# Kernel optimization log

Hardware: AMD Instinct MI355X
Metric: run time of the kernel (lower is better)

## Reference

```python
import jax, jax.numpy as jnp
import numpy as np

HEAD_NUM = 16

def setup_inputs() -> dict:
    key = jax.random.key(0)
    k1, k2 = jax.random.split(key)
    bs, seq, d = 2, 2048, 1024
    embeddings = jax.random.normal(k1, (bs, seq, d), dtype=jnp.float32)
    W = jax.random.normal(k2, (d, 3 * d), dtype=jnp.float32) * (1.0 / np.sqrt(d))
    b = jnp.zeros((3 * d,), dtype=jnp.float32)
    return {"embeddings": embeddings, "W": W, "b": b}

def reference(embeddings, W, b):
    bs, seq, d = embeddings.shape
    h = HEAD_NUM
    qkv = embeddings @ W + b                      # [b, s, 3d]
    q, k, v = jnp.split(qkv, 3, axis=-1)          # each [b, s, d]
    hd = d // h
    # Faithful to source: reshape to (bs, seq, head_dim, heads) then permute
    def split_heads(x, head_dim):
        return x.reshape(bs, seq, head_dim, h).transpose(0, 3, 1, 2)  # [b, h, s, hd]
    mq = split_heads(q, hd)
    mk = split_heads(k, hd)
    mv = split_heads(v, hd)
    scale = jnp.sqrt(jnp.asarray(hd, dtype=mq.dtype))
    scores = jnp.einsum('bhqd,bhkd->bhqk', mq, mk) / scale  # [b, h, s, s]
    attn = jax.nn.softmax(scores, axis=-1)
    out = jnp.einsum('bhqk,bhkv->bhqv', attn, mv)            # [b, h, s, hd]
    return out.transpose(0, 2, 1, 3).reshape(bs, seq, -1)    # [b, s, d]
```

## Files before the change

kernel.cpp:

```cpp
#include <hip/hip_runtime.h>
#include <stdint.h>

typedef unsigned short u16;
typedef unsigned int u32;
typedef float f32x4 __attribute__((ext_vector_type(4)));
typedef __bf16 bf16x8 __attribute__((ext_vector_type(8)));

#define BS 2
#define SEQ 2048
#define DIM 1024
#define NW3 3072
#define NH 16
#define HD 64

#define MFMA_BF16(a, b, c) __builtin_amdgcn_mfma_f32_16x16x32_bf16((a), (b), (c), 0, 0, 0)

#define GLL16(g, l)                                                                \
  __builtin_amdgcn_global_load_lds(                                                \
      (__attribute__((address_space(1))) void*)(void*)(uintptr_t)(g),              \
      (__attribute__((address_space(3))) void*)(l), 16, 0, 0)

__device__ __forceinline__ float fexp2(float x) {
#if defined(__has_builtin)
#if __has_builtin(__builtin_amdgcn_exp2f)
  return __builtin_amdgcn_exp2f(x);
#else
  return exp2f(x);
#endif
#else
  return exp2f(x);
#endif
}

__device__ __forceinline__ u16 f2bf(float x) {
  __bf16 h = (__bf16)x;
  return __builtin_bit_cast(u16, h);
}

__global__ __launch_bounds__(256) void conv_a_kernel(const float* __restrict__ A,
                                                     u16* __restrict__ O) {
  int i = (blockIdx.x * 256 + threadIdx.x) * 4;
  float4 v = *(const float4*)(A + i);
  union { u16 u[4]; ushort4 v4; } p;
  p.u[0] = f2bf(v.x); p.u[1] = f2bf(v.y); p.u[2] = f2bf(v.z); p.u[3] = f2bf(v.w);
  *(ushort4*)(O + i) = p.v4;
}

__global__ __launch_bounds__(256) void conv_wt_kernel(const float* __restrict__ W,
                                                      u16* __restrict__ Wt) {
  int id = blockIdx.x * 256 + threadIdx.x;
  int kc = id / NW3;
  int n = id - kc * NW3;
  union { u16 u[8]; uint4 v; } p;
#pragma unroll
  for (int i = 0; i < 8; ++i) p.u[i] = f2bf(W[(kc * 8 + i) * NW3 + n]);
  int h = n & 15, hd = (n & 1023) >> 4;
  int np = (n & ~1023) + h * 64 + hd;
  *(uint4*)(Wt + np * DIM + kc * 8) = p.v;
}

__global__ __launch_bounds__(256) void gemm_qkv_kernel(
    const u16* __restrict__ Ab, const u16* __restrict__ Bt, const float* __restrict__ bias,
    u16* __restrict__ Q, u16* __restrict__ K, u16* __restrict__ Vt) {
  __shared__ __align__(16) u16 Al[128 * 64];
  __shared__ __align__(16) u16 Bl[128 * 64];
  const int t = threadIdx.x;
  const int lane = t & 63, wave = t >> 6;
  const int c = lane & 15, quad = lane >> 4;
  const int tm = blockIdx.x / 24, tn = blockIdx.x - tm * 24;
  const int wm = (wave >> 1) * 64, wn = (wave & 1) * 64;

  const char* Abase = (const char*)(Ab + (size_t)tm * 128 * DIM);
  const char* Bbase = (const char*)(Bt + (size_t)tn * 128 * DIM);

  f32x4 z = {0.f, 0.f, 0.f, 0.f};
  f32x4 acc[4][4];
#pragma unroll
  for (int i = 0; i < 4; ++i)
#pragma unroll
    for (int j = 0; j < 4; ++j) acc[i][j] = z;

  for (int kt = 0; kt < 16; ++kt) {
    __syncthreads();
    const int koff = kt * 128;
#pragma unroll
    for (int r = 0; r < 4; ++r) {
      int l = r * 256 + t;
      int row = l >> 3, pos = l & 7;
      int kc = pos ^ (row & 7);
      GLL16(Abase + row * 2048 + koff + kc * 16, (char*)Al + l * 16);
      GLL16(Bbase + row * 2048 + koff + kc * 16, (char*)Bl + l * 16);
    }
    __syncthreads();
#pragma unroll
    for (int ks = 0; ks < 2; ++ks) {
      bf16x8 af[4], bfr[4];
#pragma unroll
      for (int mt = 0; mt < 4; ++mt) {
        int row = wm + mt * 16 + c;
        int kc = (ks * 4 + quad) ^ (row & 7);
        af[mt] = *(const bf16x8*)((const char*)Al + row * 128 + kc * 16);
      }
#pragma unroll
      for (int nt = 0; nt < 4; ++nt) {
        int row = wn + nt * 16 + c;
        int kc = (ks * 4 + quad) ^ (row & 7);
        bfr[nt] = *(const bf16x8*)((const char*)Bl + row * 128 + kc * 16);
      }
#pragma unroll
      for (int mt = 0; mt < 4; ++mt)
#pragma unroll
        for (int nt = 0; nt < 4; ++nt)
          acc[mt][nt] = MFMA_BF16(af[mt], bfr[nt], acc[mt][nt]);
    }
  }

#pragma unroll
  for (int nt = 0; nt < 4; ++nt) {
    int np = tn * 128 + wn + nt * 16 + c;
    int which = np >> 10;
    int rem = np & 1023;
    int h = rem >> 6, hd = rem & 63;
    float bv = bias[(np & ~1023) + hd * 16 + h];
#pragma unroll
    for (int mt = 0; mt < 4; ++mt) {
      int mbase = tm * 128 + wm + mt * 16 + quad * 4;
      int bI = mbase >> 11;
      int s0 = mbase & 2047;
      if (which == 2) {
        union { u16 u[4]; uint2 v; } p;
#pragma unroll
        for (int r = 0; r < 4; ++r) p.u[r] = f2bf(acc[mt][nt][r] + bv);
        *(uint2*)(Vt + ((size_t)(bI * NH + h) * HD + hd) * SEQ + s0) = p.v;
      } else {
        u16* dst = (which == 0) ? Q : K;
#pragma unroll
        for (int r = 0; r < 4; ++r)
          dst[((size_t)(bI * NH + h) * SEQ + (s0 + r)) * HD + hd] = f2bf(acc[mt][nt][r] + bv);
      }
    }
  }
}

#define CSC 0.18033688011112042f

#define STAGE_KV(KDST, VDST, KTILE)                                            \
  {                                                                            \
    const char* Ktb = Kb + (size_t)(KTILE) * 8192;        \
    const char* Vtb = Vb + (size_t)(KTILE) * 128;         \
    _Pragma("unroll") for (int r = 0; r < 2; ++r) {                            \
      int l = r * 256 + t;                                                     \
      int row = l >> 3, pos = l & 7;                                           \
      int kc = pos ^ (row & 7);                                                \
      GLL16(Ktb + row * 128 + kc * 16, (char*)(KDST) + l * 16);                \
      GLL16(Vtb + row * 4096 + kc * 16, (char*)(VDST) + l * 16);               \
    }                                                                          \
  }

#define COMPUTE_TILE(KT, VT)                                                   \
  {                                                                            \
    f32x4 sT[4];                                                               \
    _Pragma("unroll") for (int mt = 0; mt < 4; ++mt) {                         \
      sT[mt] = z;                                                              \
      _Pragma("unroll") for (int ks = 0; ks < 2; ++ks) {                       \
        int row = mt * 16 + c;                                                 \
        int kc = (ks * 4 + quad) ^ (row & 7);                                  \
        bf16x8 kf = *(const bf16x8*)((const char*)(KT) + row * 128 + kc * 16); \
        sT[mt] = MFMA_BF16(kf, qf[ks], sT[mt]);                                \
      }                                                                        \
    }                                                                          \
    u32 pk[4][2];                                                              \
    _Pragma("unroll") for (int mt = 0; mt < 4; ++mt) {                         \
      float p0 = fexp2(sT[mt][0] * CSC);                                       \
      float p1 = fexp2(sT[mt][1] * CSC);                                       \
      float p2 = fexp2(sT[mt][2] * CSC);                                       \
      float p3 = fexp2(sT[mt][3] * CSC);                                       \
      sm0 += p0; sm1 += p1; sm2 += p2; sm3 += p3;                              \
      pk[mt][0] = (u32)f2bf(p0) | ((u32)f2bf(p1) << 16);                       \
      pk[mt][1] = (u32)f2bf(p2) | ((u32)f2bf(p3) << 16);                       \
    }                                                                          \
    _Pragma("unroll") for (int ks = 0; ks < 2; ++ks) {                         \
      u32 a0 = __shfl(pk[2 * ks][0], sl0), a1 = __shfl(pk[2 * ks][1], sl0);    \
      u32 a2 = __shfl(pk[2 * ks][0], sl1), a3 = __shfl(pk[2 * ks][1], sl1);    \
      u32 b0 = __shfl(pk[2 * ks + 1][0], sl0);                                 \
      u32 b1 = __shfl(pk[2 * ks + 1][1], sl0);                                 \
      u32 b2 = __shfl(pk[2 * ks + 1][0], sl1);                                 \
      u32 b3 = __shfl(pk[2 * ks + 1][1], sl1);                                 \
      uint4 wv;                                                                \
      wv.x = hi ? b0 : a0; wv.y = hi ? b1 : a1;                                \
      wv.z = hi ? b2 : a2; wv.w = hi ? b3 : a3;                                \
      bf16x8 pf = __builtin_bit_cast(bf16x8, wv);                              \
      _Pragma("unroll") for (int mt = 0; mt < 4; ++mt) {                       \
        int row = mt * 16 + c;                                                 \
        int kc = (ks * 4 + quad) ^ (row & 7);                                  \
        bf16x8 vf = *(const bf16x8*)((const char*)(VT) + row * 128 + kc * 16); \
        accO[mt] = MFMA_BF16(vf, pf, accO[mt]);                                \
      }                                                                        \
    }                                                                          \
  }

__global__ __launch_bounds__(256, 4) void attn_kernel(
    const u16* __restrict__ Q, const u16* __restrict__ K,
    const u16* __restrict__ Vt, float* __restrict__ Out) {
  __shared__ __align__(16) u16 Ka[64 * 64];
  __shared__ __align__(16) u16 Kb2[64 * 64];
  __shared__ __align__(16) u16 Va[64 * 64];
  __shared__ __align__(16) u16 Vb2[64 * 64];
  const int t = threadIdx.x;
  const int lane = t & 63, wave = t >> 6;
  const int c = lane & 15, quad = lane >> 4;
  const int qt = blockIdx.x & 31, bh = blockIdx.x >> 5;
  const int h = bh & 15, b = bh >> 4;

  const u16* Qb = Q + ((size_t)bh * SEQ + qt * 64) * HD;
  const char* Kb = (const char*)(K + (size_t)bh * SEQ * HD);
  const char* Vb = (const char*)(Vt + (size_t)bh * HD * SEQ);

#pragma unroll
  for (int r = 0; r < 2; ++r) {
    int l = r * 256 + t;
    int row = l >> 3, pos = l & 7;
    int kc = pos ^ (row & 7);
    GLL16((const char*)Qb + row * 128 + kc * 16, (char*)Ka + l * 16);
  }
  __syncthreads();
  bf16x8 qf[2];
#pragma unroll
  for (int ks = 0; ks < 2; ++ks) {
    int row = wave * 16 + c;
    int kc = (ks * 4 + quad) ^ (row & 7);
    qf[ks] = *(const bf16x8*)((const char*)Ka + row * 128 + kc * 16);
  }
  __syncthreads();

  float sm0 = 0.f, sm1 = 0.f, sm2 = 0.f, sm3 = 0.f;
  f32x4 z = {0.f, 0.f, 0.f, 0.f};
  f32x4 accO[4];
#pragma unroll
  for (int i = 0; i < 4; ++i) accO[i] = z;

  const int sl0 = c + 16 * ((quad & 1) * 2);
  const int sl1 = sl0 + 16;
  const bool hi = quad >= 2;

  STAGE_KV(Ka, Va, 0);
  __syncthreads();

  for (int kt = 0; kt < 32; kt += 2) {
    STAGE_KV(Kb2, Vb2, kt + 1);
    COMPUTE_TILE(Ka, Va);
    __syncthreads();
    if (kt + 2 < 32) STAGE_KV(Ka, Va, kt + 2);
    COMPUTE_TILE(Kb2, Vb2);
    __syncthreads();
  }

  float l = (sm0 + sm1) + (sm2 + sm3);
  l += __shfl_xor(l, 16);
  l += __shfl_xor(l, 32);
  float inv = 1.f / l;
  int s = qt * 64 + wave * 16 + c;
#pragma unroll
  for (int mt = 0; mt < 4; ++mt) {
    float4 o;
    o.x = accO[mt][0] * inv;
    o.y = accO[mt][1] * inv;
    o.z = accO[mt][2] * inv;
    o.w = accO[mt][3] * inv;
    size_t off = ((size_t)(b * SEQ + s)) * DIM + h * HD + mt * 16 + quad * 4;
    *(float4*)(Out + off) = o;
  }
}

extern "C" void kernel_launch(void* const* d_in, const int* in_sizes, int n_in,
                              void* d_out, int out_size, void* d_ws, size_t ws_size,
                              hipStream_t stream) {
  (void)in_sizes; (void)n_in; (void)out_size; (void)ws_size;
  const float* emb = (const float*)d_in[0];
  const float* W = (const float*)d_in[1];
  const float* bias = (const float*)d_in[2];
  float* out = (float*)d_out;
  char* ws = (char*)d_ws;
  u16* Ab = (u16*)ws;
  u16* Wt = (u16*)(ws + 8388608);
  u16* Qd = (u16*)(ws + 14680064);
  u16* Kd = (u16*)(ws + 23068672);
  u16* Vd = (u16*)(ws + 31457280);

  conv_a_kernel<<<4096, 256, 0, stream>>>(emb, Ab);
  conv_wt_kernel<<<1536, 256, 0, stream>>>(W, Wt);
  gemm_qkv_kernel<<<768, 256, 0, stream>>>(Ab, Wt, bias, Qd, Kd, Vd);
  attn_kernel<<<1024, 256, 0, stream>>>(Qd, Kd, Vd, out);
}
```

Before: 189.7 us.

## Double-buffer QKV GEMM tiles, fuse conversion kernels, fold softmax scale into Q

The QKV GEMM now uses two LDS buffers with a K-tile of 32 and issues the load of the next tile before computing the current one. This is meant to overlap global-to-LDS traffic with MFMA work, and it halves the per-stage tile size. The two fp32-to-bf16 conversion kernels are merged into a single launch to save one launch. The softmax scale is applied to Q in the GEMM epilogue, which removes a multiply per score in the attention inner loop but rounds the scaled Q to bf16.

```diff
diff --git a/kernel.cpp b/kernel.cpp
--- a/kernel.cpp
+++ b/kernel.cpp
@@ -37,33 +37,68 @@
   return __builtin_bit_cast(u16, h);
 }
 
-__global__ __launch_bounds__(256) void conv_a_kernel(const float* __restrict__ A,
-                                                     u16* __restrict__ O) {
-  int i = (blockIdx.x * 256 + threadIdx.x) * 4;
-  float4 v = *(const float4*)(A + i);
-  union { u16 u[4]; ushort4 v4; } p;
-  p.u[0] = f2bf(v.x); p.u[1] = f2bf(v.y); p.u[2] = f2bf(v.z); p.u[3] = f2bf(v.w);
-  *(ushort4*)(O + i) = p.v4;
-}
-
-__global__ __launch_bounds__(256) void conv_wt_kernel(const float* __restrict__ W,
-                                                      u16* __restrict__ Wt) {
-  int id = blockIdx.x * 256 + threadIdx.x;
-  int kc = id / NW3;
-  int n = id - kc * NW3;
-  union { u16 u[8]; uint4 v; } p;
-#pragma unroll
-  for (int i = 0; i < 8; ++i) p.u[i] = f2bf(W[(kc * 8 + i) * NW3 + n]);
-  int h = n & 15, hd = (n & 1023) >> 4;
-  int np = (n & ~1023) + h * 64 + hd;
-  *(uint4*)(Wt + np * DIM + kc * 8) = p.v;
-}
+#define CSC 0.18033688011112042f
+
+__global__ __launch_bounds__(256) void conv_kernel(const float* __restrict__ A,
+                                                   u16* __restrict__ O,
+                                                   const float* __restrict__ W,
+                                                   u16* __restrict__ Wt) {
+  if (blockIdx.x < 4096) {
+    int i = (blockIdx.x * 256 + threadIdx.x) * 4;
+    float4 v = *(const float4*)(A + i);
+    union { u16 u[4]; ushort4 v4; } p;
+    p.u[0] = f2bf(v.x); p.u[1] = f2bf(v.y); p.u[2] = f2bf(v.z); p.u[3] = f2bf(v.w);
+    *(ushort4*)(O + i) = p.v4;
+  } else {
+    int id = (blockIdx.x - 4096) * 256 + threadIdx.x;
+    int kc = id / NW3;
+    int n = id - kc * NW3;
+    union { u16 u[8]; uint4 v; } p;
+#pragma unroll
+    for (int i = 0; i < 8; ++i) p.u[i] = f2bf(W[(kc * 8 + i) * NW3 + n]);
+    int h = n & 15, hd = (n & 1023) >> 4;
+    int np = (n & ~1023) + h * 64 + hd;
+    *(uint4*)(Wt + np * DIM + kc * 8) = p.v;
+  }
+}
+
+#define GSTAGE(ADST, BDST, KT)                                                 \
+  {                                                                            \
+    const int koff = (KT) * 64;                                \
+    _Pragma("unroll") for (int r = 0; r < 2; ++r) {                            \
+      int l = r * 256 + t;                            \
+      int row = l >> 2, pos = l & 3;                                           \
+      int kc = pos ^ (row & 3);                                                \
+      GLL16(Abase + row * 2048 + koff + kc * 16, (char*)(ADST) + l * 16);      \
+      GLL16(Bbase + row * 2048 + koff + kc * 16, (char*)(BDST) + l * 16);      \
+    }                                                                          \
+  }
+
+#define GCOMPUTE(AT, BT)                                                       \
+  {                                                                            \
+    bf16x8 af[4], bfr[4];                                                      \
+    _Pragma("unroll") for (int mt = 0; mt < 4; ++mt) {                         \
+      int row = wm + mt * 16 + c;                                              \
+      int kc = quad ^ (row & 3);                                               \
+      af[mt] = *(const bf16x8*)((const char*)(AT) + row * 64 + kc * 16);       \
+    }                                                                          \
+    _Pragma("unroll") for (int nt = 0; nt < 4; ++nt) {                         \
+      int row = wn + nt * 16 + c;                                              \
+      int kc = quad ^ (row & 3);                                               \
+      bfr[nt] = *(const bf16x8*)((const char*)(BT) + row * 64 + kc * 16);      \
+    }                                                                          \
+    _Pragma("unroll") for (int mt = 0; mt < 4; ++mt)                           \
+      _Pragma("unroll") for (int nt = 0; nt < 4; ++nt)                         \
+        acc[mt][nt] = MFMA_BF16(af[mt], bfr[nt], acc[mt][nt]);                 \
+  }
 
 __global__ __launch_bounds__(256) void gemm_qkv_kernel(
     const u16* __restrict__ Ab, const u16* __restrict__ Bt, const float* __restrict__ bias,
     u16* __restrict__ Q, u16* __restrict__ K, u16* __restrict__ Vt) {
-  __shared__ __align__(16) u16 Al[128 * 64];
-  __shared__ __align__(16) u16 Bl[128 * 64];
+  __shared__ __align__(16) u16 Aa[128 * 32];
+  __shared__ __align__(16) u16 Ab2[128 * 32];
+  __shared__ __align__(16) u16 Ba[128 * 32];
+  __shared__ __align__(16) u16 Bb2[128 * 32];
   const int t = threadIdx.x;
   const int lane = t & 63, wave = t >> 6;
   const int c = lane & 15, quad = lane >> 4;
@@ -80,39 +115,15 @@
 #pragma unroll
     for (int j = 0; j < 4; ++j) acc[i][j] = z;
 
-  for (int kt = 0; kt < 16; ++kt) {
+  GSTAGE(Aa, Ba, 0);
+  __syncthreads();
+  for (int kt = 0; kt < 32; kt += 2) {
+    GSTAGE(Ab2, Bb2, kt + 1);
+    GCOMPUTE(Aa, Ba);
     __syncthreads();
-    const int koff = kt * 128;
-#pragma unroll
-    for (int r = 0; r < 4; ++r) {
-      int l = r * 256 + t;
-      int row = l >> 3, pos = l & 7;
-      int kc = pos ^ (row & 7);
-      GLL16(Abase + row * 2048 + koff + kc * 16, (char*)Al + l * 16);
-      GLL16(Bbase + row * 2048 + koff + kc * 16, (char*)Bl + l * 16);
-    }
+    if (kt + 2 < 32) GSTAGE(Aa, Ba, kt + 2);
+    GCOMPUTE(Ab2, Bb2);
     __syncthreads();
-#pragma unroll
-    for (int ks = 0; ks < 2; ++ks) {
-      bf16x8 af[4], bfr[4];
-#pragma unroll
-      for (int mt = 0; mt < 4; ++mt) {
-        int row = wm + mt * 16 + c;
-        int kc = (ks * 4 + quad) ^ (row & 7);
-        af[mt] = *(const bf16x8*)((const char*)Al + row * 128 + kc * 16);
-      }
-#pragma unroll
-      for (int nt = 0; nt < 4; ++nt) {
-        int row = wn + nt * 16 + c;
-        int kc = (ks * 4 + quad) ^ (row & 7);
-        bfr[nt] = *(const bf16x8*)((const char*)Bl + row * 128 + kc * 16);
-      }
-#pragma unroll
-      for (int mt = 0; mt < 4; ++mt)
-#pragma unroll
-        for (int nt = 0; nt < 4; ++nt)
-          acc[mt][nt] = MFMA_BF16(af[mt], bfr[nt], acc[mt][nt]);
-    }
   }
 
 #pragma unroll
@@ -122,6 +133,8 @@
     int rem = np & 1023;
     int h = rem >> 6, hd = rem & 63;
     float bv = bias[(np & ~1023) + hd * 16 + h];
+    float sc = (which == 0) ? CSC : 1.0f;
+    float bvs = bv * sc;
 #pragma unroll
     for (int mt = 0; mt < 4; ++mt) {
       int mbase = tm * 128 + wm + mt * 16 + quad * 4;
@@ -136,13 +149,12 @@
         u16* dst = (which == 0) ? Q : K;
 #pragma unroll
         for (int r = 0; r < 4; ++r)
-          dst[((size_t)(bI * NH + h) * SEQ + (s0 + r)) * HD + hd] = f2bf(acc[mt][nt][r] + bv);
+          dst[((size_t)(bI * NH + h) * SEQ + (s0 + r)) * HD + hd] =
+              f2bf(acc[mt][nt][r] * sc + bvs);
       }
     }
   }
 }
-
-#define CSC 0.18033688011112042f
 
 #define STAGE_KV(KDST, VDST, KTILE)                                            \
   {                                                                            \
@@ -171,10 +183,10 @@
     }                                                                          \
     u32 pk[4][2];                                                              \
     _Pragma("unroll") for (int mt = 0; mt < 4; ++mt) {                         \
-      float p0 = fexp2(sT[mt][0] * CSC);                                       \
-      float p1 = fexp2(sT[mt][1] * CSC);                                       \
-      float p2 = fexp2(sT[mt][2] * CSC);                                       \
-      float p3 = fexp2(sT[mt][3] * CSC);                                       \
+      float p0 = fexp2(sT[mt][0]);                                             \
+      float p1 = fexp2(sT[mt][1]);                                             \
+      float p2 = fexp2(sT[mt][2]);                                             \
+      float p3 = fexp2(sT[mt][3]);                                             \
       sm0 += p0; sm1 += p1; sm2 += p2; sm3 += p3;                              \
       pk[mt][0] = (u32)f2bf(p0) | ((u32)f2bf(p1) << 16);                       \
       pk[mt][1] = (u32)f2bf(p2) | ((u32)f2bf(p3) << 16);                       \
@@ -287,8 +299,7 @@
   u16* Kd = (u16*)(ws + 23068672);
   u16* Vd = (u16*)(ws + 31457280);
 
-  conv_a_kernel<<<4096, 256, 0, stream>>>(emb, Ab);
-  conv_wt_kernel<<<1536, 256, 0, stream>>>(W, Wt);
+  conv_kernel<<<5632, 256, 0, stream>>>(emb, Ab, W, Wt);
   gemm_qkv_kernel<<<768, 256, 0, stream>>>(Ab, Wt, bias, Qd, Kd, Vd);
   attn_kernel<<<1024, 256, 0, stream>>>(Qd, Kd, Vd, out);
 }
```

Result: faster. 179.1 us (-5.6%).
